# Performance work log

Measured on AMD Instinct MI355X. Metric: run time of the kernel, lower is better.

## Reference

```python
import jax, jax.numpy as jnp
import numpy as np

N_NODES = 100000
N_EDGES = 1600000
IN_FEATS = 64
OUT_FEATS = 64


def setup_inputs() -> dict:
    key = jax.random.key(0)
    k1, k2, k3, k4 = jax.random.split(key, 4)
    features = jax.random.normal(k1, (N_NODES, IN_FEATS), dtype=jnp.float32)
    src = jax.random.randint(k2, (N_EDGES,), 0, N_NODES, dtype=jnp.int32)
    dst = jax.random.randint(k3, (N_EDGES,), 0, N_NODES, dtype=jnp.int32)
    # Linear(in_feats, out_feats): W is [out, in] like torch, b is [out]
    W = jax.random.normal(k4, (OUT_FEATS, IN_FEATS), dtype=jnp.float32) * (1.0 / np.sqrt(IN_FEATS))
    b = jnp.zeros((OUT_FEATS,), dtype=jnp.float32)
    return {"features": features, "src": src, "dst": dst, "W": W, "b": b}


def reference(features, src, dst, W, b):
    # update_all(copy_src('h','m'), sum('m','h')): for each edge, message = h[src],
    # aggregated by sum at dst. Equivalent to a segment-sum scatter-add.
    msgs = features[src]  # [E, in_feats] gather
    agg = jax.ops.segment_sum(msgs, dst, num_segments=N_NODES)  # [N, in_feats]
    # NodeUpdateModule: Linear + relu (dropout=0 so no dropout path)
    h = jnp.einsum('ni,oi->no', agg, W) + b
    return jax.nn.relu(h)
```

## Files before the change

### kernel.cpp

```cpp
#include <hip/hip_runtime.h>

#define N_NODES 100000
#define N_EDGES 1600000
#define TILES 6250

#define NPB 128
#define NB 782
#define SUBS 256
#define CAP 14
#define OVF_CAP 16384u
#define LOVF_CAP 512
#define LISTCAP 3712
#define GEMM_BLKS 98

typedef __attribute__((ext_vector_type(8))) short short8;
typedef __attribute__((ext_vector_type(4))) float f32x4;

static __device__ __forceinline__ unsigned short f2bf(float f) {
    unsigned int u = __float_as_uint(f);
    unsigned int r = (u + 0x7fffu + ((u >> 16) & 1u)) >> 16;
    return (unsigned short)r;
}
static __device__ __forceinline__ float bfl(unsigned int u) {
    return __uint_as_float(u << 16);
}
static __device__ __forceinline__ float bfh(unsigned int u) {
    return __uint_as_float(u & 0xffff0000u);
}

__global__ __launch_bounds__(1024) void gcn_prep(
    const float* __restrict__ feat, const float* __restrict__ W,
    unsigned int* __restrict__ g32,
    const int* __restrict__ src, const int* __restrict__ dst,
    unsigned int* __restrict__ cursor, unsigned int* __restrict__ region,
    unsigned int* __restrict__ ovf_cnt, uint2* __restrict__ ovf) {
    __shared__ unsigned int cnt[NB];
    __shared__ unsigned int data[NB][CAP];
    __shared__ uint2 lovf[LOVF_CAP];
    __shared__ unsigned int lovf_n, lovf_base;

    int tid = threadIdx.x;
    if (blockIdx.x >= SUBS) {
        int b = blockIdx.x - SUBS;
        int l = tid & 63, wv = tid >> 6;
        int r = l & 15, c = l >> 4;

        short8 bfr[4][2];
#pragma unroll
        for (int t = 0; t < 4; ++t)
#pragma unroll
            for (int s = 0; s < 2; ++s) {
                const float* wp = W + (16 * t + r) * 64 + 32 * s + c * 8;
                float4 w0 = *(const float4*)wp;
                float4 w1 = *(const float4*)(wp + 4);
                short8 f;
                f[0] = (short)f2bf(w0.x); f[1] = (short)f2bf(w0.y);
                f[2] = (short)f2bf(w0.z); f[3] = (short)f2bf(w0.w);
                f[4] = (short)f2bf(w1.x); f[5] = (short)f2bf(w1.y);
                f[6] = (short)f2bf(w1.z); f[7] = (short)f2bf(w1.w);
                bfr[t][s] = f;
            }

        int tile0 = (b * 16 + wv) * 4;
#pragma unroll
        for (int ti = 0; ti < 4; ++ti) {
            int tile = tile0 + ti;
            if (tile >= TILES) break;
            int m0 = tile * 16;
            f32x4 acc0 = {0,0,0,0}, acc1 = {0,0,0,0}, acc2 = {0,0,0,0}, acc3 = {0,0,0,0};
#pragma unroll
            for (int s = 0; s < 2; ++s) {
                const float* ap = feat + (m0 + r) * 64 + 32 * s + c * 8;
                float4 a0 = *(const float4*)ap;
                float4 a1 = *(const float4*)(ap + 4);
                short8 af;
                af[0] = (short)f2bf(a0.x); af[1] = (short)f2bf(a0.y);
                af[2] = (short)f2bf(a0.z); af[3] = (short)f2bf(a0.w);
                af[4] = (short)f2bf(a1.x); af[5] = (short)f2bf(a1.y);
                af[6] = (short)f2bf(a1.z); af[7] = (short)f2bf(a1.w);
                acc0 = __builtin_amdgcn_mfma_f32_16x16x32_bf16(af, bfr[0][s], acc0, 0, 0, 0);
                acc1 = __builtin_amdgcn_mfma_f32_16x16x32_bf16(af, bfr[1][s], acc1, 0, 0, 0);
                acc2 = __builtin_amdgcn_mfma_f32_16x16x32_bf16(af, bfr[2][s], acc2, 0, 0, 0);
                acc3 = __builtin_amdgcn_mfma_f32_16x16x32_bf16(af, bfr[3][s], acc3, 0, 0, 0);
            }
#pragma unroll
            for (int t = 0; t < 4; ++t) {
                f32x4 a = (t == 0) ? acc0 : (t == 1) ? acc1 : (t == 2) ? acc2 : acc3;
#pragma unroll
                for (int reg = 0; reg < 4; ++reg) {
                    float dv = a[reg];
                    float o = __shfl_xor(dv, 1);
                    if (!(l & 1)) {
                        int m = m0 + c * 4 + reg;
                        int n = 16 * t + r;
                        g32[(m * 64 + n) >> 1] =
                            (unsigned int)f2bf(dv) | ((unsigned int)f2bf(o) << 16);
                    }
                }
            }
        }
        return;
    }

    int sub = blockIdx.x;
    for (int i = tid; i < NB; i += 1024) cnt[i] = 0;
    if (tid == 0) lovf_n = 0;
    __syncthreads();

    int base = sub * (N_EDGES / SUBS);
    int end = base + (N_EDGES / SUBS);
    int i = base + tid;
    int s = 0, d = 0;
    if (i < end) { s = src[i]; d = dst[i]; }
    while (i < end) {
        int inext = i + 1024;
        int sn = 0, dn = 0;
        if (inext < end) { sn = src[inext]; dn = dst[inext]; }
        int bk = d >> 7;
        unsigned int c = atomicAdd(&cnt[bk], 1u);
        if (c < CAP) {
            data[bk][c] = ((unsigned int)(d & 127) << 17) | (unsigned int)s;
        } else {
            unsigned int o = atomicAdd(&lovf_n, 1u);
            if (o < LOVF_CAP) lovf[o] = make_uint2((unsigned int)s, (unsigned int)d);
        }
        i = inext; s = sn; d = dn;
    }
    __syncthreads();

    unsigned int rbase = (unsigned int)sub * NB * CAP;
    for (int idx = tid; idx < NB * CAP; idx += 1024) {
        int bk = idx / CAP, slot = idx - bk * CAP;
        unsigned int c = cnt[bk];
        if (slot < (int)(c < CAP ? c : CAP))
            region[rbase + (unsigned int)idx] = data[bk][slot];
    }
    for (int bk = tid; bk < NB; bk += 1024)
        cursor[sub * NB + bk] = cnt[bk];

    unsigned int n = lovf_n < LOVF_CAP ? lovf_n : LOVF_CAP;
    if (tid == 0) lovf_base = atomicAdd(ovf_cnt, n);
    __syncthreads();
    for (unsigned int t = tid; t < n; t += 1024) {
        unsigned int p = lovf_base + t;
        if (p < OVF_CAP) ovf[p] = lovf[t];
    }
}

__global__ __launch_bounds__(512, 8) void gcn_gather3(
    const uint2* __restrict__ g64, const unsigned int* __restrict__ cursor,
    const unsigned int* __restrict__ region, const unsigned int* __restrict__ ovf_cnt,
    const uint2* __restrict__ ovf, const float* __restrict__ bias,
    float* __restrict__ out) {
    __shared__ unsigned int sorted[LISTCAP];
    __shared__ unsigned int scnt[SUBS];
    __shared__ unsigned int cnt2[NPB], off2[NPB], cur2[NPB];

    int b = blockIdx.x;
    int tid = threadIdx.x;

    if (tid < SUBS) {
        unsigned int c = cursor[(unsigned)tid * NB + b];
        scnt[tid] = c < CAP ? c : CAP;
    }
    if (tid < NPB) cnt2[tid] = 0;
    __syncthreads();

    for (int idx = tid; idx < SUBS * CAP; idx += 512) {
        int s = idx / CAP, slot = idx - s * CAP;
        if (slot < (int)scnt[s]) {
            unsigned int v =
                __builtin_nontemporal_load(&region[((unsigned)s * NB + b) * CAP + slot]);
            atomicAdd(&cnt2[v >> 17], 1u);
        }
    }
    unsigned int oc = *ovf_cnt;
    if (oc > OVF_CAP) oc = OVF_CAP;
    for (unsigned int i = tid; i < oc; i += 512) {
        uint2 e = ovf[i];
        if ((int)(e.y >> 7) == b) atomicAdd(&cnt2[e.y & 127u], 1u);
    }
    __syncthreads();

    if (tid < NPB) off2[tid] = cnt2[tid];
    __syncthreads();
    for (int off = 1; off < NPB; off <<= 1) {
        unsigned int t = 0;
        if (tid < NPB && tid >= off) t = off2[tid - off];
        __syncthreads();
        if (tid < NPB) off2[tid] += t;
        __syncthreads();
    }
    if (tid < NPB) cur2[tid] = off2[tid] - cnt2[tid];
    __syncthreads();

    for (int idx = tid; idx < SUBS * CAP; idx += 512) {
        int s = idx / CAP, slot = idx - s * CAP;
        if (slot < (int)scnt[s]) {
            unsigned int v = region[((unsigned)s * NB + b) * CAP + slot];
            unsigned int p = atomicAdd(&cur2[v >> 17], 1u);
            if (p < LISTCAP) sorted[p] = v & 0x1FFFFu;
        }
    }
    for (unsigned int i = tid; i < oc; i += 512) {
        uint2 e = ovf[i];
        if ((int)(e.y >> 7) == b) {
            unsigned int p = atomicAdd(&cur2[e.y & 127u], 1u);
            if (p < LISTCAP) sorted[p] = e.x;
        }
    }
    __syncthreads();

    int wv = tid >> 6, l = tid & 63, grp = l >> 4, k = l & 15;
#pragma unroll
    for (int nb = 0; nb < 4; ++nb) {
        int dl = wv * 16 + nb * 4 + grp;
        int node = b * NPB + dl;
        if (node < N_NODES) {
            unsigned int start = off2[dl] - cnt2[dl];
            int cnt = (int)cnt2[dl];
            float a0 = 0.f, a1 = 0.f, a2 = 0.f, a3 = 0.f;
#pragma unroll 8
            for (int j = 0; j < cnt; ++j) {
                unsigned int s0 = sorted[start + j];
                uint2 w = g64[s0 * 16 + k];
                a0 += bfl(w.x); a1 += bfh(w.x); a2 += bfl(w.y); a3 += bfh(w.y);
            }
            float4 b4 = *(const float4*)(bias + 4 * k);
            f32x4 o;
            o.x = fmaxf(a0 + b4.x, 0.0f);
            o.y = fmaxf(a1 + b4.y, 0.0f);
            o.z = fmaxf(a2 + b4.z, 0.0f);
            o.w = fmaxf(a3 + b4.w, 0.0f);
            __builtin_nontemporal_store(o, (f32x4*)(out + node * 64 + 4 * k));
        }
    }
}

extern "C" void kernel_launch(void* const* d_in, const int* in_sizes, int n_in,
                              void* d_out, int out_size, void* d_ws, size_t ws_size,
                              hipStream_t stream) {
    const float* features = (const float*)d_in[0];
    const int*   src      = (const int*)d_in[1];
    const int*   dst      = (const int*)d_in[2];
    const float* W        = (const float*)d_in[3];
    const float* b        = (const float*)d_in[4];
    float* out = (float*)d_out;

    unsigned int* ws     = (unsigned int*)d_ws;
    unsigned int* cursor = ws;
    unsigned int* ovfcnt = ws + 200192;
    uint2*        ovf    = (uint2*)(ws + 200256);
    unsigned int* region = ws + 233024;
    unsigned int* g32    = ws + 3035712;

    (void)hipMemsetAsync(ovfcnt, 0, 64 * sizeof(unsigned int), stream);

    gcn_prep<<<SUBS + GEMM_BLKS, 1024, 0, stream>>>(
        features, W, g32, src, dst, cursor, region, ovfcnt, ovf);
    gcn_gather3<<<NB, 512, 0, stream>>>((const uint2*)g32, cursor, region,
                                        ovfcnt, ovf, b, out);
}
```

Baseline: 86.59 us.

## Split gather blocks into half-buckets with ballot-compacted edge lists

The gather kernel now launches two 256-thread blocks per 128-node bucket, each handling 64 destination nodes. Each block reads the bucket's region once, keeps only its half's edges in a shared list using wave ballot compaction, then counts and sorts from that list instead of rereading region and overflow memory. This doubles the block count to improve occupancy and load balance and drops the second global pass, at the cost of each region being read by two blocks and an extra shared-memory staging step. LISTCAP is halved, so a half-bucket with more than 1792 edges would be silently truncated.

```diff
diff --git a/kernel.cpp b/kernel.cpp
--- a/kernel.cpp
+++ b/kernel.cpp
@@ -10,7 +10,7 @@
 #define CAP 14
 #define OVF_CAP 16384u
 #define LOVF_CAP 512
-#define LISTCAP 3712
+#define LISTCAP 1792
 #define GEMM_BLKS 98
 
 typedef __attribute__((ext_vector_type(8))) short short8;
@@ -147,75 +147,85 @@
     }
 }
 
-__global__ __launch_bounds__(512, 8) void gcn_gather3(
+__global__ __launch_bounds__(256) void gcn_gather4(
     const uint2* __restrict__ g64, const unsigned int* __restrict__ cursor,
     const unsigned int* __restrict__ region, const unsigned int* __restrict__ ovf_cnt,
     const uint2* __restrict__ ovf, const float* __restrict__ bias,
     float* __restrict__ out) {
+    __shared__ unsigned int list[LISTCAP];
     __shared__ unsigned int sorted[LISTCAP];
     __shared__ unsigned int scnt[SUBS];
-    __shared__ unsigned int cnt2[NPB], off2[NPB], cur2[NPB];
-
-    int b = blockIdx.x;
+    __shared__ unsigned int cnt2[64], off2[64], cur2[64];
+    __shared__ unsigned int ln;
+
+    int b = blockIdx.x >> 1;
+    unsigned int half = blockIdx.x & 1;
     int tid = threadIdx.x;
+    int lane = tid & 63;
 
     if (tid < SUBS) {
         unsigned int c = cursor[(unsigned)tid * NB + b];
         scnt[tid] = c < CAP ? c : CAP;
     }
-    if (tid < NPB) cnt2[tid] = 0;
-    __syncthreads();
-
-    for (int idx = tid; idx < SUBS * CAP; idx += 512) {
+    if (tid < 64) cnt2[tid] = 0;
+    if (tid == 0) ln = 0;
+    __syncthreads();
+
+    for (int idx = tid; idx < SUBS * CAP; idx += 256) {
         int s = idx / CAP, slot = idx - s * CAP;
+        unsigned int v = 0;
+        bool mine = false;
         if (slot < (int)scnt[s]) {
-            unsigned int v =
-                __builtin_nontemporal_load(&region[((unsigned)s * NB + b) * CAP + slot]);
-            atomicAdd(&cnt2[v >> 17], 1u);
+            v = region[((unsigned)s * NB + b) * CAP + slot];
+            mine = (v >> 23) == half;
+        }
+        unsigned long long mask = __ballot(mine);
+        unsigned int base = 0;
+        if (lane == 0) base = atomicAdd(&ln, (unsigned int)__popcll(mask));
+        base = __shfl(base, 0);
+        if (mine) {
+            unsigned int p = base + (unsigned int)__popcll(mask & ((1ull << lane) - 1ull));
+            if (p < LISTCAP) list[p] = v;
         }
     }
     unsigned int oc = *ovf_cnt;
     if (oc > OVF_CAP) oc = OVF_CAP;
-    for (unsigned int i = tid; i < oc; i += 512) {
+    for (unsigned int i = tid; i < oc; i += 256) {
         uint2 e = ovf[i];
-        if ((int)(e.y >> 7) == b) atomicAdd(&cnt2[e.y & 127u], 1u);
-    }
-    __syncthreads();
-
-    if (tid < NPB) off2[tid] = cnt2[tid];
-    __syncthreads();
-    for (int off = 1; off < NPB; off <<= 1) {
+        if ((e.y >> 7) == (unsigned int)b && ((e.y >> 6) & 1u) == half) {
+            unsigned int p = atomicAdd(&ln, 1u);
+            if (p < LISTCAP) list[p] = ((e.y & 127u) << 17) | e.x;
+        }
+    }
+    __syncthreads();
+    unsigned int T = ln < LISTCAP ? ln : LISTCAP;
+
+    for (unsigned int i = tid; i < T; i += 256)
+        atomicAdd(&cnt2[(list[i] >> 17) & 63u], 1u);
+    __syncthreads();
+    if (tid < 64) off2[tid] = cnt2[tid];
+    __syncthreads();
+    for (int off = 1; off < 64; off <<= 1) {
         unsigned int t = 0;
-        if (tid < NPB && tid >= off) t = off2[tid - off];
+        if (tid < 64 && tid >= off) t = off2[tid - off];
         __syncthreads();
-        if (tid < NPB) off2[tid] += t;
+        if (tid < 64) off2[tid] += t;
         __syncthreads();
     }
-    if (tid < NPB) cur2[tid] = off2[tid] - cnt2[tid];
-    __syncthreads();
-
-    for (int idx = tid; idx < SUBS * CAP; idx += 512) {
-        int s = idx / CAP, slot = idx - s * CAP;
-        if (slot < (int)scnt[s]) {
-            unsigned int v = region[((unsigned)s * NB + b) * CAP + slot];
-            unsigned int p = atomicAdd(&cur2[v >> 17], 1u);
-            if (p < LISTCAP) sorted[p] = v & 0x1FFFFu;
-        }
-    }
-    for (unsigned int i = tid; i < oc; i += 512) {
-        uint2 e = ovf[i];
-        if ((int)(e.y >> 7) == b) {
-            unsigned int p = atomicAdd(&cur2[e.y & 127u], 1u);
-            if (p < LISTCAP) sorted[p] = e.x;
-        }
-    }
-    __syncthreads();
-
-    int wv = tid >> 6, l = tid & 63, grp = l >> 4, k = l & 15;
+    if (tid < 64) cur2[tid] = off2[tid] - cnt2[tid];
+    __syncthreads();
+    for (unsigned int i = tid; i < T; i += 256) {
+        unsigned int v = list[i];
+        unsigned int p = atomicAdd(&cur2[(v >> 17) & 63u], 1u);
+        if (p < LISTCAP) sorted[p] = v & 0x1FFFFu;
+    }
+    __syncthreads();
+
+    int wv = tid >> 6, grp = lane >> 4, k = lane & 15;
 #pragma unroll
     for (int nb = 0; nb < 4; ++nb) {
         int dl = wv * 16 + nb * 4 + grp;
-        int node = b * NPB + dl;
+        int node = b * NPB + (int)half * 64 + dl;
         if (node < N_NODES) {
             unsigned int start = off2[dl] - cnt2[dl];
             int cnt = (int)cnt2[dl];
@@ -258,6 +268,6 @@
 
     gcn_prep<<<SUBS + GEMM_BLKS, 1024, 0, stream>>>(
         features, W, g32, src, dst, cursor, region, ovfcnt, ovf);
-    gcn_gather3<<<NB, 512, 0, stream>>>((const uint2*)g32, cursor, region,
-                                        ovfcnt, ovf, b, out);
-}
+    gcn_gather4<<<NB * 2, 256, 0, stream>>>((const uint2*)g32, cursor, region,
+                                            ovfcnt, ovf, b, out);
+}
```

Result: no change. 85.48 us (-1.3%).
